# Kernel tuning notes

Measured on AMD Instinct MI355X. Metric: run time of the kernel, lower is better.

## Reference

```python
import jax, jax.numpy as jnp
import numpy as np

D = 2048   # embed_dim
E = 128    # expand_ratio = head dim
H = D // E # num heads = 16
C = 64     # chunk size for the chunked linear-attention scan
EPS = 1e-6


def setup_inputs() -> dict:
    key = jax.random.key(0)
    ks = jax.random.split(key, 6)
    b, n = 2, 2048
    s = 0.02
    x = jax.random.normal(ks[0], (b, n, D), jnp.float32)
    Wq = (jax.random.normal(ks[1], (D, D), jnp.float32) * s)
    Wk = (jax.random.normal(ks[2], (D, D), jnp.float32) * s)
    Wv = (jax.random.normal(ks[3], (D, D), jnp.float32) * s)
    Wf = (jax.random.normal(ks[4], (D, H), jnp.float32) * s)
    Wo = (jax.random.normal(ks[5], (D, D), jnp.float32) * s)
    norm_w = jnp.ones((D,), jnp.float32)
    return {"x": x, "Wq": Wq, "Wk": Wk, "Wv": Wv, "Wf": Wf, "Wo": Wo, "norm_w": norm_w}


def _lightning_scalar_decay(q, k, v, ld):
    # q,k,v: [b,n,H,E], ld: [b,n,H] log decay per head per step.
    # Recurrence: S_t = exp(ld_t) * S_{t-1} + k_t^T v_t ; o_t = q_t @ S_t
    b, n, h, e = q.shape
    nc = n // C
    qc = q.reshape(b, nc, C, h, e)
    kc = k.reshape(b, nc, C, h, e)
    vc = v.reshape(b, nc, C, h, e)
    ldc = ld.reshape(b, nc, C, h)
    cum = jnp.cumsum(ldc, axis=2)          # inclusive within-chunk log decay [b,nc,C,h]
    tot = cum[:, :, -1, :]                 # [b,nc,h]

    # intra-chunk: scores[i,j] = (q_i . k_j) * exp(L_i - L_j), j <= i
    Lh = cum.transpose(0, 1, 3, 2)         # [b,nc,h,C]
    decay = jnp.exp(Lh[..., :, None] - Lh[..., None, :])  # [b,nc,h,C,C]
    mask = jnp.tril(jnp.ones((C, C), bool))
    scores = jnp.einsum('bmihe,bmjhe->bmhij', qc, kc) * decay
    scores = jnp.where(mask, scores, 0.0)
    o_intra = jnp.einsum('bmhij,bmjhe->bmihe', scores, vc)

    # inter-chunk: carried recurrent state S [b,h,e,e]
    def step(S, inp):
        q_c, k_c, v_c, cum_c, tot_c = inp  # [b,C,h,e],...,[b,C,h],[b,h]
        o = jnp.einsum('bihe,bhef->bihf', q_c * jnp.exp(cum_c)[..., None], S)
        kd = k_c * jnp.exp(tot_c[:, None, :] - cum_c)[..., None]
        S_new = S * jnp.exp(tot_c)[:, :, None, None] + jnp.einsum('bihe,bihf->bhef', kd, v_c)
        return S_new, o

    xs = (qc.transpose(1, 0, 2, 3, 4), kc.transpose(1, 0, 2, 3, 4),
          vc.transpose(1, 0, 2, 3, 4), cum.transpose(1, 0, 2, 3), tot.transpose(1, 0, 2))
    S0 = jnp.zeros((b, h, e, e), q.dtype)
    S_final, o_inter = jax.lax.scan(step, S0, xs)
    o_inter = o_inter.transpose(1, 0, 2, 3, 4)  # [b,nc,C,h,e]
    return (o_intra + o_inter).reshape(b, n, h * e), S_final


def reference(x, Wq, Wk, Wv, Wf, Wo, norm_w):
    b, n, d = x.shape
    q = jax.nn.silu(x @ Wq).reshape(b, n, H, E)
    k = jax.nn.silu(x @ Wk).reshape(b, n, H, E)
    v = (x @ Wv).reshape(b, n, H, E)
    ld = jax.nn.log_sigmoid(x @ Wf)  # [b,n,H]
    o, _ = _lightning_scalar_decay(q, k, v, ld)
    # RMSNorm over full embed dim
    o = o * jax.lax.rsqrt(jnp.mean(o * o, axis=-1, keepdims=True) + EPS) * norm_w
    return o @ Wo
```

## Files before the change

### kernel.cpp

```cpp
#include <hip/hip_runtime.h>
#include <hip/hip_bf16.h>
#include <stdint.h>

#define D_ 2048
#define E_ 128
#define H_ 16
#define NB_ 2
#define NSEQ_ 2048
#define NTOK_ 4096
#define NCH_ 32

typedef short bf16s;
typedef __attribute__((ext_vector_type(8))) short bf16x8;
typedef __attribute__((ext_vector_type(4))) float f32x4;

__device__ __forceinline__ short f2b(float f) {
  __hip_bfloat16 h = __float2bfloat16(f);
  return *reinterpret_cast<short*>(&h);
}
__device__ __forceinline__ float b2f(short s) {
  __hip_bfloat16 h;
  *reinterpret_cast<short*>(&h) = s;
  return __bfloat162float(h);
}

__device__ __forceinline__ void gload_lds16(const void* g, void* l) {
  __builtin_amdgcn_global_load_lds(
      (__attribute__((address_space(1))) void*)(const_cast<void*>(g)),
      (__attribute__((address_space(3))) void*)(l), 16, 0, 0);
}

template <int N>
__device__ __forceinline__ void wait_vmcnt() {
  if constexpr (N == 0)      asm volatile("s_waitcnt vmcnt(0)" ::: "memory");
  else if constexpr (N == 6) asm volatile("s_waitcnt vmcnt(6)" ::: "memory");
  else static_assert(N == 0, "unsupported vmcnt");
}
__device__ __forceinline__ void lgkm0_fence() {
  asm volatile("s_waitcnt lgkmcnt(0)" ::: "memory");
  __builtin_amdgcn_sched_barrier(0);
}

__global__ __launch_bounds__(256)
void cvt_bf16(const float* __restrict__ x, bf16s* __restrict__ y) {
  const size_t i = (size_t)blockIdx.x * 256 + threadIdx.x;
  const float4 a = ((const float4*)x)[i * 2];
  const float4 b = ((const float4*)x)[i * 2 + 1];
  bf16x8 o;
  o[0] = f2b(a.x); o[1] = f2b(a.y); o[2] = f2b(a.z); o[3] = f2b(a.w);
  o[4] = f2b(b.x); o[5] = f2b(b.y); o[6] = f2b(b.z); o[7] = f2b(b.w);
  *(bf16x8*)&y[i * 8] = o;
}

__global__ __launch_bounds__(256)
void transpose_w(const float* __restrict__ Wq, const float* __restrict__ Wk,
                 const float* __restrict__ Wv, const float* __restrict__ Wo,
                 const float* __restrict__ nw, bf16s* __restrict__ WqT,
                 bf16s* __restrict__ WkT, bf16s* __restrict__ WvT,
                 bf16s* __restrict__ WoT) {
  const float* src; bf16s* dst;
  if (blockIdx.z == 0)      { src = Wq; dst = WqT; }
  else if (blockIdx.z == 1) { src = Wk; dst = WkT; }
  else if (blockIdx.z == 2) { src = Wv; dst = WvT; }
  else                      { src = Wo; dst = WoT; }
  __shared__ float tile[64][65];
  const int n0 = blockIdx.x * 64, k0 = blockIdx.y * 64;
  const int t = threadIdx.x;
  const int tr = t >> 6, tc = t & 63;
#pragma unroll
  for (int rr = 0; rr < 16; ++rr) {
    const int row = rr * 4 + tr;
    tile[row][tc] = src[(size_t)(k0 + row) * D_ + n0 + tc];
  }
  __syncthreads();
  const float wk = (blockIdx.z == 3) ? nw[k0 + tc] : 1.f;
#pragma unroll
  for (int rr = 0; rr < 16; ++rr) {
    const int row = rr * 4 + tr;
    dst[(size_t)(n0 + row) * D_ + k0 + tc] = f2b(tile[tc][row] * wk);
  }
}

__global__ __launch_bounds__(256)
void ld_gemm(const float* __restrict__ x, const float* __restrict__ Wf,
             float* __restrict__ ldb) {
  const int t = threadIdx.x;
  const int col = t & 15;
  const int tok = blockIdx.x * 16 + (t >> 4);
  const float4* xr = (const float4*)(x + (size_t)tok * D_);
  float s = 0.f;
#pragma unroll 4
  for (int kk = 0; kk < D_ / 4; ++kk) {
    const float4 xv = xr[kk];
    const int k4 = kk * 4;
    s += xv.x * Wf[(k4 + 0) * H_ + col];
    s += xv.y * Wf[(k4 + 1) * H_ + col];
    s += xv.z * Wf[(k4 + 2) * H_ + col];
    s += xv.w * Wf[(k4 + 3) * H_ + col];
  }
  const float m = fminf(s, 0.f);
  ldb[(size_t)tok * H_ + col] = m - log1pf(__expf(-fabsf(s)));
}

__global__ __launch_bounds__(512, 2)
void gemm_qkv8p(const bf16s* __restrict__ xb, const bf16s* __restrict__ WqT,
                const bf16s* __restrict__ WkT, const bf16s* __restrict__ WvT,
                bf16s* __restrict__ qb, bf16s* __restrict__ kb,
                bf16s* __restrict__ vb) {
  const int bn = blockIdx.x, bm = blockIdx.y, z = blockIdx.z;
  const bf16s* Bt; bf16s* outp; int act;
  if (z == 0)      { Bt = WqT; outp = qb; act = 1; }
  else if (z == 1) { Bt = WkT; outp = kb; act = 1; }
  else             { Bt = WvT; outp = vb; act = 0; }

  __shared__ bf16s As[2 * 256 * 64];
  __shared__ bf16s Bs[2 * 256 * 64];
  const int t = threadIdx.x;
  const int w = t >> 6, l = t & 63;
  const int wm = w >> 2, wn = w & 3;
  const int lr = l & 15, lk = l >> 4;

  const size_t abase = (size_t)(bm * 256) * D_;
  const size_t bbase = (size_t)(bn * 256) * D_;

  f32x4 acc[8][4] = {};

  auto stageHT = [&](int m, int part) {
    const int slot = m & 1;
    const int k0 = m * 64;
    const int rowoff = (part >> 1) * 128;
    const bool isB = part & 1;
    const bf16s* g = isB ? Bt : xb;
    const size_t gb = (isB ? bbase : abase) + (size_t)rowoff * D_ + k0;
    bf16s* lb = (isB ? Bs : As) + slot * (256 * 64) + rowoff * 64;
#pragma unroll
    for (int rr = 0; rr < 2; ++rr) {
      const int r = rr * 64 + (t >> 3);
      const int cs = (t & 7) ^ (r & 7);
      gload_lds16(&g[gb + (size_t)r * D_ + cs * 8], &lb[rr * 4096 + w * 512]);
    }
  };
  auto ldA = [&](int slot, int fm, int ks) -> bf16x8 {
    const int row = fm * 32 + wm * 16 + lr;
    return *(const bf16x8*)&As[slot * (256 * 64) + row * 64 +
                               (((ks << 2) + lk) ^ (row & 7)) * 8];
  };
  auto ldB = [&](int slot, int fn, int ks) -> bf16x8 {
    const int row = fn * 64 + wn * 16 + lr;
    return *(const bf16x8*)&Bs[slot * (256 * 64) + row * 64 +
                               (((ks << 2) + lk) ^ (row & 7)) * 8];
  };

  stageHT(0, 0); stageHT(0, 1); stageHT(0, 2); stageHT(0, 3);
  stageHT(1, 0); stageHT(1, 1); stageHT(1, 2);
  wait_vmcnt<6>();
  __builtin_amdgcn_s_barrier();

  bf16x8 af[4][2], bf0[2][2], bf1[2][2];
  for (int j = 0; j < 32; ++j) {
    const int s = j & 1;
#pragma unroll
    for (int fm = 0; fm < 4; ++fm)
#pragma unroll
      for (int ks = 0; ks < 2; ++ks) af[fm][ks] = ldA(s, fm, ks);
#pragma unroll
    for (int fn = 0; fn < 2; ++fn)
#pragma unroll
      for (int ks = 0; ks < 2; ++ks) bf0[fn][ks] = ldB(s, fn, ks);
    if (j <= 30) stageHT(j + 1, 3);
    __builtin_amdgcn_s_barrier();
    lgkm0_fence();
    __builtin_amdgcn_s_setprio(1);
#pragma unroll
    for (int fm = 0; fm < 4; ++fm)
#pragma unroll
      for (int fn = 0; fn < 2; ++fn)
#pragma unroll
        for (int ks = 0; ks < 2; ++ks)
          acc[fm][fn] = __builtin_amdgcn_mfma_f32_16x16x32_bf16(
              af[fm][ks], bf0[fn][ks], acc[fm][fn], 0, 0, 0);
    __builtin_amdgcn_s_setprio(0);
    __builtin_amdgcn_s_barrier();
#pragma unroll
    for (int fn = 0; fn < 2; ++fn)
#pragma unroll
      for (int ks = 0; ks < 2; ++ks) bf1[fn][ks] = ldB(s, fn + 2, ks);
    if (j <= 29) stageHT(j + 2, 0);
    __builtin_amdgcn_s_barrier();
    lgkm0_fence();
    __builtin_amdgcn_s_setprio(1);
#pragma unroll
    for (int fm = 0; fm < 4; ++fm)
#pragma unroll
      for (int fn = 0; fn < 2; ++fn)
#pragma unroll
        for (int ks = 0; ks < 2; ++ks)
          acc[fm][fn + 2] = __builtin_amdgcn_mfma_f32_16x16x32_bf16(
              af[fm][ks], bf1[fn][ks], acc[fm][fn + 2], 0, 0, 0);
    __builtin_amdgcn_s_setprio(0);
    __builtin_amdgcn_s_barrier();
#pragma unroll
    for (int fm = 0; fm < 4; ++fm)
#pragma unroll
      for (int ks = 0; ks < 2; ++ks) af[fm][ks] = ldA(s, fm + 4, ks);
    if (j <= 29) stageHT(j + 2, 1);
    __builtin_amdgcn_s_barrier();
    lgkm0_fence();
    __builtin_amdgcn_s_setprio(1);
#pragma unroll
    for (int fm = 0; fm < 4; ++fm)
#pragma unroll
      for (int fn = 0; fn < 2; ++fn)
#pragma unroll
        for (int ks = 0; ks < 2; ++ks)
          acc[fm + 4][fn + 2] = __builtin_amdgcn_mfma_f32_16x16x32_bf16(
              af[fm][ks], bf1[fn][ks], acc[fm + 4][fn + 2], 0, 0, 0);
    __builtin_amdgcn_s_setprio(0);
    __builtin_amdgcn_s_barrier();
    if (j <= 29) stageHT(j + 2, 2);
    __builtin_amdgcn_s_setprio(1);
#pragma unroll
    for (int fm = 0; fm < 4; ++fm)
#pragma unroll
      for (int fn = 0; fn < 2; ++fn)
#pragma unroll
        for (int ks = 0; ks < 2; ++ks)
          acc[fm + 4][fn] = __builtin_amdgcn_mfma_f32_16x16x32_bf16(
              af[fm][ks], bf0[fn][ks], acc[fm + 4][fn], 0, 0, 0);
    __builtin_amdgcn_s_setprio(0);
    if (j <= 29)      wait_vmcnt<6>();
    else if (j == 30) wait_vmcnt<0>();
    __builtin_amdgcn_s_barrier();
  }

#pragma unroll
  for (int fm = 0; fm < 8; ++fm) {
    const int row = bm * 256 + fm * 32 + wm * 16 + lk * 4;
#pragma unroll
    for (int fn = 0; fn < 4; ++fn) {
      const int col = bn * 256 + fn * 64 + wn * 16 + lr;
#pragma unroll
      for (int r = 0; r < 4; ++r) {
        float vv = acc[fm][fn][r];
        if (act) vv = vv / (1.f + __expf(-vv));
        outp[(size_t)(row + r) * D_ + col] = f2b(vv);
      }
    }
  }
}

__device__ __forceinline__ void gemm_body128(const bf16s* __restrict__ A,
                                             const bf16s* __restrict__ Bt,
                                             float* __restrict__ Cm, int bm,
                                             int bn, const float* __restrict__ rs) {
  constexpr int BK = 64;
  __shared__ bf16s As[128 * BK];
  __shared__ bf16s Bs[128 * BK];
  const int t = threadIdx.x;
  const int w = t >> 6, l = t & 63;
  const int wm = w >> 1, wn = w & 1;
  const int lr = l & 15, lk = l >> 4;
  const int sr8 = l >> 3, sc = l & 7;
  const int cs = sc ^ sr8;
  f32x4 acc[4][4] = {};

  const size_t abase = (size_t)(bm * 128) * D_;
  const size_t bbase = (size_t)(bn * 128) * D_;

  for (int k0 = 0; k0 < D_; k0 += BK) {
    __syncthreads();
#pragma unroll
    for (int j = 0; j < 4; ++j) {
      const int row = w * 32 + j * 8;
      gload_lds16(&A[abase + (size_t)(row + sr8) * D_ + k0 + cs * 8],
                  &As[row * BK]);
      gload_lds16(&Bt[bbase + (size_t)(row + sr8) * D_ + k0 + cs * 8],
                  &Bs[row * BK]);
    }
    __syncthreads();
    bf16x8 af[4][2], bfr[4][2];
#pragma unroll
    for (int tm = 0; tm < 4; ++tm) {
      const int row = wm * 64 + tm * 16 + lr;
#pragma unroll
      for (int ks = 0; ks < 2; ++ks)
        af[tm][ks] =
            *(const bf16x8*)&As[row * BK + ((ks * 4 + lk) ^ (row & 7)) * 8];
    }
#pragma unroll
    for (int tn = 0; tn < 4; ++tn) {
      const int row = wn * 64 + tn * 16 + lr;
#pragma unroll
      for (int ks = 0; ks < 2; ++ks)
        bfr[tn][ks] =
            *(const bf16x8*)&Bs[row * BK + ((ks * 4 + lk) ^ (row & 7)) * 8];
    }
#pragma unroll
    for (int ks = 0; ks < 2; ++ks)
#pragma unroll
      for (int tm = 0; tm < 4; ++tm)
#pragma unroll
        for (int tn = 0; tn < 4; ++tn)
          acc[tm][tn] = __builtin_amdgcn_mfma_f32_16x16x32_bf16(
              af[tm][ks], bfr[tn][ks], acc[tm][tn], 0, 0, 0);
  }

#pragma unroll
  for (int tm = 0; tm < 4; ++tm) {
    const int rowb = bm * 128 + wm * 64 + tm * 16 + lk * 4;
#pragma unroll
    for (int tn = 0; tn < 4; ++tn) {
      const int col = bn * 128 + wn * 64 + tn * 16 + lr;
#pragma unroll
      for (int r = 0; r < 4; ++r) {
        float vv = acc[tm][tn][r] * rs[rowb + r];
        Cm[(size_t)(rowb + r) * D_ + col] = vv;
      }
    }
  }
}

__global__ __launch_bounds__(256)
void gemm_out(const bf16s* __restrict__ A, const bf16s* __restrict__ Bt,
              const float* __restrict__ rs, float* __restrict__ out) {
  const int orig = blockIdx.x;
  const int lin = (orig & 7) * 64 + (orig >> 3);
  const int bm = lin & 31;
  const int bn = lin >> 5;
  gemm_body128(A, Bt, out, bm, bn, rs);
}

__global__ __launch_bounds__(256)
void chunk_state(const bf16s* __restrict__ k, const bf16s* __restrict__ v,
                 const float* __restrict__ ldp, bf16s* __restrict__ Mbuf,
                 float* __restrict__ totb) {
  const int c = blockIdx.x, bh = blockIdx.y;
  const int b = bh >> 4, h = bh & 15;
  const int t = threadIdx.x;
  const int w = t >> 6, l = t & 63;
  const int lr = l & 15, lk = l >> 4;

  __shared__ bf16s Kt[64 * 128];
  __shared__ bf16s Vn[64 * 128];
  __shared__ bf16s KdT[128 * 64];
  __shared__ bf16s VtT[128 * 64];
  __shared__ float cumS[64];
  char* cKt = (char*)Kt; char* cVn = (char*)Vn;
  char* cKdT = (char*)KdT; char* cVtT = (char*)VtT;

  const size_t grow0 = (size_t)b * NSEQ_ + c * 64;
#pragma unroll
  for (int j = 0; j < 4; ++j) {
    const int lrow = w * 16 + j * 4 + (l >> 4);
    const int ck = (l & 15) ^ (lrow & 7);
    const size_t goff = (grow0 + lrow) * D_ + h * E_ + ck * 8;
    const int lbase = (w * 16 + j * 4) * 128;
    gload_lds16(&k[goff], &Kt[lbase]);
    gload_lds16(&v[goff], &Vn[lbase]);
  }
  if (w == 0) {
    float val = ldp[(grow0 + l) * H_ + h];
#pragma unroll
    for (int off = 1; off < 64; off <<= 1) {
      float pv = __shfl_up(val, off);
      if (l >= off) val += pv;
    }
    cumS[l] = val;
  }
  __syncthreads();
  const float tot = cumS[63];
  if (t == 0) totb[bh * NCH_ + c] = tot;

#pragma unroll
  for (int it = 0; it < 4; ++it) {
    const int task = t + it * 256;
    const int i = task >> 4, cx = task & 15;
    const int sb = i * 256 + ((cx * 16) ^ ((i & 7) << 4));
    bf16x8 vv = *(const bf16x8*)(cVn + sb);
    bf16x8 kk8 = *(const bf16x8*)(cKt + sb);
    const float sE = __expf(tot - cumS[i]);
#pragma unroll
    for (int jj = 0; jj < 8; ++jj) {
      const int e = cx * 8 + jj;
      const int db = e * 128 + ((i * 2) ^ ((e & 7) << 4));
      *(bf16s*)(cVtT + db) = vv[jj];
      *(bf16s*)(cKdT + db) = f2b(b2f(kk8[jj]) * sE);
    }
  }
  __syncthreads();

  const int wm = w >> 1, wn = w & 1;
  f32x4 acc[4][4] = {};
#pragma unroll
  for (int kk2 = 0; kk2 < 2; ++kk2) {
    const int cb = (kk2 * 32 + lk * 8) * 2;
    bf16x8 af[4], bfr[4];
#pragma unroll
    for (int tm = 0; tm < 4; ++tm) {
      const int fr = wm * 64 + tm * 16 + lr;
      af[tm] = *(const bf16x8*)(cVtT + fr * 128 + (cb ^ ((fr & 7) << 4)));
    }
#pragma unroll
    for (int tn = 0; tn < 4; ++tn) {
      const int er = wn * 64 + tn * 16 + lr;
      bfr[tn] = *(const bf16x8*)(cKdT + er * 128 + (cb ^ ((er & 7) << 4)));
    }
#pragma unroll
    for (int tm = 0; tm < 4; ++tm)
#pragma unroll
      for (int tn = 0; tn < 4; ++tn)
        acc[tm][tn] = __builtin_amdgcn_mfma_f32_16x16x32_bf16(
            af[tm], bfr[tn], acc[tm][tn], 0, 0, 0);
  }
  const size_t mb = (size_t)(bh * NCH_ + c) * 128 * 128;
#pragma unroll
  for (int tm = 0; tm < 4; ++tm) {
#pragma unroll
    for (int tn = 0; tn < 4; ++tn) {
#pragma unroll
      for (int r = 0; r < 4; ++r) {
        const int f = wm * 64 + tm * 16 + lk * 4 + r;
        const int e = wn * 64 + tn * 16 + lr;
        Mbuf[mb + f * 128 + e] = f2b(acc[tm][tn][r]);
      }
    }
  }
}

__global__ __launch_bounds__(256)
void state_scan(const bf16s* __restrict__ Mbuf, const float* __restrict__ totb,
                bf16s* __restrict__ Sbuf) {
  const int sl = blockIdx.x;
  const int bh = blockIdx.y;
  const int t = threadIdx.x;
  const int fr = sl * 16 + (t >> 4);
  const int e0 = (t & 15) * 8;
  const size_t base = ((size_t)(bh * NCH_) * 128 + fr) * 128 + e0;
  const size_t cstride = 128 * 128;
  __shared__ float tots[NCH_];
  if (t < NCH_) tots[t] = totb[bh * NCH_ + t];
  __syncthreads();
  float acc[8] = {};
  bf16x8 m0 = *(const bf16x8*)&Mbuf[base + 0 * cstride];
  bf16x8 m1 = *(const bf16x8*)&Mbuf[base + 1 * cstride];
  bf16x8 m2 = *(const bf16x8*)&Mbuf[base + 2 * cstride];
  bf16x8 m3 = *(const bf16x8*)&Mbuf[base + 3 * cstride];
#pragma unroll
  for (int c = 0; c < NCH_; ++c) {
    bf16x8 sv;
#pragma unroll
    for (int j = 0; j < 8; ++j) sv[j] = f2b(acc[j]);
    *(bf16x8*)&Sbuf[base + (size_t)c * cstride] = sv;
    const bf16x8 mc = ((c & 3) == 0) ? m0 : ((c & 3) == 1) ? m1
                     : ((c & 3) == 2) ? m2 : m3;
    const float dt = __expf(tots[c]);
#pragma unroll
    for (int j = 0; j < 8; ++j) acc[j] = acc[j] * dt + b2f(mc[j]);
    if (c + 4 < NCH_) {
      const bf16x8 mn = *(const bf16x8*)&Mbuf[base + (size_t)(c + 4) * cstride];
      if ((c & 3) == 0) m0 = mn;
      else if ((c & 3) == 1) m1 = mn;
      else if ((c & 3) == 2) m2 = mn;
      else m3 = mn;
    }
  }
}

__global__ __launch_bounds__(256)
void attn_out(const bf16s* __restrict__ q, const bf16s* __restrict__ k,
              const bf16s* __restrict__ v, const float* __restrict__ ldp,
              const bf16s* __restrict__ Sbuf, bf16s* __restrict__ o) {
  const int c = blockIdx.x, bh = blockIdx.y;
  const int b = bh >> 4, h = bh & 15;
  const int t = threadIdx.x;
  const int w = t >> 6, l = t & 63;
  const int lr = l & 15, lk = l >> 4;

  __shared__ bf16s Qt[64 * 128];
  __shared__ bf16s Kt[64 * 128];
  __shared__ bf16s Vn[64 * 128];
  __shared__ bf16s VtT[128 * 64];
  __shared__ bf16s Pm[64 * 64];
  __shared__ float cumS[64];
  char* cQt = (char*)Qt; char* cKt = (char*)Kt; char* cVn = (char*)Vn;
  char* cVtT = (char*)VtT; char* cPm = (char*)Pm;

  const size_t grow0 = (size_t)b * NSEQ_ + c * 64;
  const size_t sbase = (size_t)(bh * NCH_ + c) * 128 * 128;
  const bf16x8* Sp = (const bf16x8*)&Sbuf[sbase];
#pragma unroll
  for (int j = 0; j < 4; ++j) {
    const int lrow = w * 16 + j * 4 + (l >> 4);
    const int ck = (l & 15) ^ (lrow & 7);
    const size_t goff = (grow0 + lrow) * D_ + h * E_ + ck * 8;
    const int lbase = (w * 16 + j * 4) * 128;
    gload_lds16(&q[goff], &Qt[lbase]);
    gload_lds16(&k[goff], &Kt[lbase]);
    gload_lds16(&v[goff], &Vn[lbase]);
  }
  if (w == 0) {
    float val = ldp[(grow0 + l) * H_ + h];
#pragma unroll
    for (int off = 1; off < 64; off <<= 1) {
      float pv = __shfl_up(val, off);
      if (l >= off) val += pv;
    }
    cumS[l] = val;
  }
  __syncthreads();

#pragma unroll
  for (int it = 0; it < 4; ++it) {
    const int task = t + it * 256;
    const int i = task >> 4, cx = task & 15;
    const int sb = i * 256 + ((cx * 16) ^ ((i & 7) << 4));
    bf16x8 vv = *(const bf16x8*)(cVn + sb);
#pragma unroll
    for (int jj = 0; jj < 8; ++jj) {
      const int e = cx * 8 + jj;
      const int db = e * 128 + ((i * 2) ^ ((e & 7) << 4));
      *(bf16s*)(cVtT + db) = vv[jj];
    }
  }

  f32x4 accs[4] = {};
  f32x4 acco[8] = {};
#pragma unroll
  for (int kk = 0; kk < 4; ++kk) {
    const int cb = (kk * 32 + lk * 8) * 2;
    const int ar = w * 16 + lr;
    bf16x8 aq = *(const bf16x8*)(cQt + ar * 256 + (cb ^ ((ar & 7) << 4)));
#pragma unroll
    for (int tn = 0; tn < 4; ++tn) {
      const int br = tn * 16 + lr;
      bf16x8 bk = *(const bf16x8*)(cKt + br * 256 + (cb ^ ((br & 7) << 4)));
      accs[tn] = __builtin_amdgcn_mfma_f32_16x16x32_bf16(aq, bk, accs[tn], 0, 0, 0);
    }
#pragma unroll
    for (int tf = 0; tf < 8; ++tf) {
      bf16x8 bs = Sp[(tf * 16 + lr) * 16 + kk * 4 + lk];
      acco[tf] = __builtin_amdgcn_mfma_f32_16x16x32_bf16(aq, bs, acco[tf], 0, 0, 0);
    }
  }
#pragma unroll
  for (int r = 0; r < 4; ++r) {
    const float gI = __expf(cumS[w * 16 + lk * 4 + r]);
#pragma unroll
    for (int tf = 0; tf < 8; ++tf) acco[tf][r] *= gI;
  }
#pragma unroll
  for (int tn = 0; tn < 4; ++tn) {
    const int j = tn * 16 + lr;
    const float cj = cumS[j];
#pragma unroll
    for (int r = 0; r < 4; ++r) {
      const int i = w * 16 + lk * 4 + r;
      const float sv = (j <= i) ? accs[tn][r] * __expf(cumS[i] - cj) : 0.f;
      *(bf16s*)(cPm + i * 128 + ((j * 2) ^ ((i & 7) << 4))) = f2b(sv);
    }
  }
  __syncthreads();

#pragma unroll
  for (int kk2 = 0; kk2 < 2; ++kk2) {
    const int cb = (kk2 * 32 + lk * 8) * 2;
    const int pr = w * 16 + lr;
    bf16x8 ap = *(const bf16x8*)(cPm + pr * 128 + (cb ^ ((pr & 7) << 4)));
#pragma unroll
    for (int tf = 0; tf < 8; ++tf) {
      const int fr = tf * 16 + lr;
      bf16x8 bv = *(const bf16x8*)(cVtT + fr * 128 + (cb ^ ((fr & 7) << 4)));
      acco[tf] = __builtin_amdgcn_mfma_f32_16x16x32_bf16(ap, bv, acco[tf], 0, 0, 0);
    }
  }
#pragma unroll
  for (int tf = 0; tf < 8; ++tf) {
#pragma unroll
    for (int r = 0; r < 4; ++r) {
      const int i = w * 16 + lk * 4 + r;
      o[(grow0 + i) * D_ + h * E_ + tf * 16 + lr] = f2b(acco[tf][r]);
    }
  }
}

__global__ __launch_bounds__(256)
void rms_scale(const bf16s* __restrict__ o, float* __restrict__ sout) {
  const int tok = blockIdx.x;
  const int t = threadIdx.x;
  bf16x8 vv = *(const bf16x8*)&o[(size_t)tok * D_ + t * 8];
  float s = 0.f;
#pragma unroll
  for (int j = 0; j < 8; ++j) { const float f = b2f(vv[j]); s += f * f; }
#pragma unroll
  for (int off2 = 32; off2 > 0; off2 >>= 1) s += __shfl_down(s, off2);
  __shared__ float wsum[4];
  if ((t & 63) == 0) wsum[t >> 6] = s;
  __syncthreads();
  if (t == 0)
    sout[tok] = rsqrtf((wsum[0] + wsum[1] + wsum[2] + wsum[3]) * (1.f / D_) +
                       1e-6f);
}

extern "C" void kernel_launch(void* const* d_in, const int* in_sizes, int n_in,
                              void* d_out, int out_size, void* d_ws,
                              size_t ws_size, hipStream_t stream) {
  (void)in_sizes; (void)n_in; (void)out_size;
  const float* x  = (const float*)d_in[0];
  const float* Wq = (const float*)d_in[1];
  const float* Wk = (const float*)d_in[2];
  const float* Wv = (const float*)d_in[3];
  const float* Wf = (const float*)d_in[4];
  const float* Wo = (const float*)d_in[5];
  const float* nw = (const float*)d_in[6];
  float* out = (float*)d_out;

  char* ws = (char*)d_ws;
  const size_t MB = 1024 * 1024;
  bf16s* xb   = (bf16s*)(ws + 0);
  bf16s* WqT  = (bf16s*)(ws + 16 * MB);
  bf16s* WkT  = (bf16s*)(ws + 24 * MB);
  bf16s* WvT  = (bf16s*)(ws + 32 * MB);
  bf16s* Sbuf = (bf16s*)(ws + 0);
  float* totb = (float*)(ws + 32 * MB);
  bf16s* WoT  = (bf16s*)(ws + 40 * MB);
  bf16s* qb   = (bf16s*)(ws + 48 * MB);
  bf16s* kb   = (bf16s*)(ws + 64 * MB);
  bf16s* vb   = (bf16s*)(ws + 80 * MB);
  bf16s* ob   = (bf16s*)(ws + 96 * MB);
  bf16s* Mbuf = (bf16s*)(ws + 112 * MB);
  float* ldb  = (float*)(ws + 144 * MB);
  float* rsb  = (float*)(ws + 145 * MB);
  if (146 * MB > ws_size) return;

  cvt_bf16<<<NTOK_ * D_ / 8 / 256, 256, 0, stream>>>(x, xb);
  transpose_w<<<dim3(32, 32, 4), 256, 0, stream>>>(Wq, Wk, Wv, Wo, nw, WqT,
                                                   WkT, WvT, WoT);
  ld_gemm<<<NTOK_ / 16, 256, 0, stream>>>(x, Wf, ldb);
  gemm_qkv8p<<<dim3(8, 16, 3), 512, 0, stream>>>(xb, WqT, WkT, WvT, qb, kb, vb);
  chunk_state<<<dim3(NCH_, NB_ * H_), 256, 0, stream>>>(kb, vb, ldb, Mbuf, totb);
  state_scan<<<dim3(8, NB_ * H_), 256, 0, stream>>>(Mbuf, totb, Sbuf);
  attn_out<<<dim3(NCH_, NB_ * H_), 256, 0, stream>>>(qb, kb, vb, ldb, Sbuf, ob);
  rms_scale<<<NTOK_, 256, 0, stream>>>(ob, rsb);
  gemm_out<<<512, 256, 0, stream>>>(ob, WoT, rsb, out);
}
```

Before: 299.3 us.

## Restructure GEMM main loop from four phases to two per k-tile

Collapses the projection GEMM's 4-phase ping-pong schedule into 2 phases. Each phase now loads twice the fragments, issues two stage copies and runs 32 MFMAs. The prefetch depth and vmcnt threshold are adjusted to match. This halves the barriers and waits per k-step, at the cost of more live fragment registers and a different load/compute overlap pattern.

```diff
diff --git a/kernel.cpp b/kernel.cpp
--- a/kernel.cpp
+++ b/kernel.cpp
@@ -33,7 +33,7 @@
 template <int N>
 __device__ __forceinline__ void wait_vmcnt() {
   if constexpr (N == 0)      asm volatile("s_waitcnt vmcnt(0)" ::: "memory");
-  else if constexpr (N == 6) asm volatile("s_waitcnt vmcnt(6)" ::: "memory");
+  else if constexpr (N == 4) asm volatile("s_waitcnt vmcnt(4)" ::: "memory");
   else static_assert(N == 0, "unsupported vmcnt");
 }
 __device__ __forceinline__ void lgkm0_fence() {
@@ -152,8 +152,8 @@
   };
 
   stageHT(0, 0); stageHT(0, 1); stageHT(0, 2); stageHT(0, 3);
-  stageHT(1, 0); stageHT(1, 1); stageHT(1, 2);
-  wait_vmcnt<6>();
+  stageHT(1, 0); stageHT(1, 1);
+  wait_vmcnt<4>();
   __builtin_amdgcn_s_barrier();
 
   bf16x8 af[4][2], bf0[2][2], bf1[2][2];
@@ -166,8 +166,11 @@
 #pragma unroll
     for (int fn = 0; fn < 2; ++fn)
 #pragma unroll
-      for (int ks = 0; ks < 2; ++ks) bf0[fn][ks] = ldB(s, fn, ks);
-    if (j <= 30) stageHT(j + 1, 3);
+      for (int ks = 0; ks < 2; ++ks) {
+        bf0[fn][ks] = ldB(s, fn, ks);
+        bf1[fn][ks] = ldB(s, fn + 2, ks);
+      }
+    if (j <= 30) { stageHT(j + 1, 3); stageHT(j + 1, 2); }
     __builtin_amdgcn_s_barrier();
     lgkm0_fence();
     __builtin_amdgcn_s_setprio(1);
@@ -176,16 +179,19 @@
 #pragma unroll
       for (int fn = 0; fn < 2; ++fn)
 #pragma unroll
-        for (int ks = 0; ks < 2; ++ks)
+        for (int ks = 0; ks < 2; ++ks) {
           acc[fm][fn] = __builtin_amdgcn_mfma_f32_16x16x32_bf16(
               af[fm][ks], bf0[fn][ks], acc[fm][fn], 0, 0, 0);
+          acc[fm][fn + 2] = __builtin_amdgcn_mfma_f32_16x16x32_bf16(
+              af[fm][ks], bf1[fn][ks], acc[fm][fn + 2], 0, 0, 0);
+        }
     __builtin_amdgcn_s_setprio(0);
     __builtin_amdgcn_s_barrier();
 #pragma unroll
-    for (int fn = 0; fn < 2; ++fn)
-#pragma unroll
-      for (int ks = 0; ks < 2; ++ks) bf1[fn][ks] = ldB(s, fn + 2, ks);
-    if (j <= 29) stageHT(j + 2, 0);
+    for (int fm = 0; fm < 4; ++fm)
+#pragma unroll
+      for (int ks = 0; ks < 2; ++ks) af[fm][ks] = ldA(s, fm + 4, ks);
+    if (j <= 29) { stageHT(j + 2, 0); stageHT(j + 2, 1); }
     __builtin_amdgcn_s_barrier();
     lgkm0_fence();
     __builtin_amdgcn_s_setprio(1);
@@ -194,41 +200,14 @@
 #pragma unroll
       for (int fn = 0; fn < 2; ++fn)
 #pragma unroll
-        for (int ks = 0; ks < 2; ++ks)
-          acc[fm][fn + 2] = __builtin_amdgcn_mfma_f32_16x16x32_bf16(
-              af[fm][ks], bf1[fn][ks], acc[fm][fn + 2], 0, 0, 0);
-    __builtin_amdgcn_s_setprio(0);
-    __builtin_amdgcn_s_barrier();
-#pragma unroll
-    for (int fm = 0; fm < 4; ++fm)
-#pragma unroll
-      for (int ks = 0; ks < 2; ++ks) af[fm][ks] = ldA(s, fm + 4, ks);
-    if (j <= 29) stageHT(j + 2, 1);
-    __builtin_amdgcn_s_barrier();
-    lgkm0_fence();
-    __builtin_amdgcn_s_setprio(1);
-#pragma unroll
-    for (int fm = 0; fm < 4; ++fm)
-#pragma unroll
-      for (int fn = 0; fn < 2; ++fn)
-#pragma unroll
-        for (int ks = 0; ks < 2; ++ks)
+        for (int ks = 0; ks < 2; ++ks) {
           acc[fm + 4][fn + 2] = __builtin_amdgcn_mfma_f32_16x16x32_bf16(
               af[fm][ks], bf1[fn][ks], acc[fm + 4][fn + 2], 0, 0, 0);
-    __builtin_amdgcn_s_setprio(0);
-    __builtin_amdgcn_s_barrier();
-    if (j <= 29) stageHT(j + 2, 2);
-    __builtin_amdgcn_s_setprio(1);
-#pragma unroll
-    for (int fm = 0; fm < 4; ++fm)
-#pragma unroll
-      for (int fn = 0; fn < 2; ++fn)
-#pragma unroll
-        for (int ks = 0; ks < 2; ++ks)
           acc[fm + 4][fn] = __builtin_amdgcn_mfma_f32_16x16x32_bf16(
               af[fm][ks], bf0[fn][ks], acc[fm + 4][fn], 0, 0, 0);
+        }
     __builtin_amdgcn_s_setprio(0);
-    if (j <= 29)      wait_vmcnt<6>();
+    if (j <= 29)      wait_vmcnt<4>();
     else if (j == 30) wait_vmcnt<0>();
     __builtin_amdgcn_s_barrier();
   }
```

Result: no change. 298.8 us (-0.1%).
